# Performance work log

Measured on AMD Instinct MI355X. Metric: run time of the kernel, lower is better.

Reference implementation:

```python
import jax, jax.numpy as jnp
import numpy as np

NUM_HEADS = 16
ROPE_THETA = 10000.0


def _vision_rope_tables(seq_len, head_dim):
    # Llama4 vision ('mllama4') 2D rotary: x/y patch-grid positions,
    # interleaved (non-neox) complex pairs. Returns cos/sin [S, head_dim//2].
    idx = int(np.sqrt(seq_len))  # patches per side (24 for 336/14)
    pos = np.arange(seq_len)
    fx = (pos % idx + 1).astype(np.float32)
    fy = (pos // idx + 1).astype(np.float32)
    freq_dim = head_dim // 2
    rope_freq = 1.0 / ROPE_THETA ** (
        np.arange(0, freq_dim, 2)[: freq_dim // 2].astype(np.float32) / freq_dim
    )
    fx = np.repeat(fx[:, None] * rope_freq[None, :], 2, axis=-1)  # [S, freq_dim]
    fy = np.repeat(fy[:, None] * rope_freq[None, :], 2, axis=-1)
    freqs = np.concatenate([fx, fy], axis=-1)[:, ::2]  # [S, head_dim//2]
    return jnp.asarray(np.cos(freqs)), jnp.asarray(np.sin(freqs))


def _apply_rope(x, cos, sin):
    # x: [B, S, H, D]; even/odd interleaved pairs treated as complex numbers
    B, S, H, D = x.shape
    xr = x.reshape(B, S, H, D // 2, 2)
    x0, x1 = xr[..., 0], xr[..., 1]
    c = cos[None, :, None, :]
    s = sin[None, :, None, :]
    o0 = x0 * c - x1 * s
    o1 = x0 * s + x1 * c
    return jnp.stack([o0, o1], axis=-1).reshape(B, S, H, D)


def setup_inputs() -> dict:
    key = jax.random.key(0)
    ks = jax.random.split(key, 5)
    E = 1408
    B, S = 16, 576
    scale = 0.02
    return {
        "hidden_states": jax.random.normal(ks[0], (B, S, E), dtype=jnp.float32),
        "w_qkv": jax.random.normal(ks[1], (E, 3 * E), dtype=jnp.float32) * scale,
        "b_qkv": jax.random.normal(ks[2], (3 * E,), dtype=jnp.float32) * scale,
        "w_o": jax.random.normal(ks[3], (E, E), dtype=jnp.float32) * scale,
        "b_o": jax.random.normal(ks[4], (E,), dtype=jnp.float32) * scale,
    }


def reference(hidden_states, w_qkv, b_qkv, w_o, b_o):
    B, S, E = hidden_states.shape
    H = NUM_HEADS
    D = E // H
    scaling = D ** -0.5

    qkv = hidden_states @ w_qkv + b_qkv  # [B,S,3E]
    q, k, v = jnp.split(qkv, 3, axis=-1)
    q = q.reshape(B, S, H, D)
    k = k.reshape(B, S, H, D)
    v = v.reshape(B, S, H, D)

    cos, sin = _vision_rope_tables(S, D)
    q = _apply_rope(q, cos, sin)
    k = _apply_rope(k, cos, sin)

    q = q * scaling
    scores = jnp.einsum("bqhd,bkhd->bhqk", q, k)  # full bidirectional attention
    probs = jax.nn.softmax(scores, axis=-1)
    attn = jnp.einsum("bhqk,bkhd->bqhd", probs, v).reshape(B, S, E)

    return attn @ w_o + b_o
```

## Files before the change

kernel.cpp:

```cpp
#include <hip/hip_runtime.h>
#include <hip/hip_bf16.h>


typedef unsigned short UST;
typedef __attribute__((ext_vector_type(8))) __bf16 bf16x8;
typedef __attribute__((ext_vector_type(4))) float f32x4;
typedef __attribute__((ext_vector_type(8))) UST us8;
typedef __attribute__((ext_vector_type(4))) UST us4;

typedef __attribute__((address_space(3))) unsigned int lds_u32;
typedef const __attribute__((address_space(1))) unsigned int glob_u32;

static __device__ __forceinline__ float bf2f(UST u){
  unsigned int x = ((unsigned int)u) << 16;
  return __builtin_bit_cast(float, x);
}
static __device__ __forceinline__ UST f2bf(float f){
  unsigned int x = __builtin_bit_cast(unsigned int, f);
  x += 0x7fffu + ((x >> 16) & 1u);
  return (UST)(x >> 16);
}

__global__ void k_tables(float* __restrict__ cs2){
  int s = blockIdx.x;
  int p = threadIdx.x;
  if (p >= 44) return;
  int tt = p % 22;
  double comp = (p < 22) ? (double)(s % 24 + 1) : (double)(s / 24 + 1);
  double a = comp * pow(10000.0, -(double)tt / 22.0);
  cs2[s*88 + 2*p]     = (float)cos(a);
  cs2[s*88 + 2*p + 1] = (float)sin(a);
}

__global__ void k_zero(UST* __restrict__ qa, UST* __restrict__ ka, UST* __restrict__ vt){
  int c = blockIdx.x*256 + threadIdx.x;
  int bh = c / 576, s = c - bh*576;
  us8 z = {0,0,0,0,0,0,0,0};
  *(us8*)(qa + ((size_t)bh*576 + s)*96 + 88) = z;
  *(us8*)(ka + ((size_t)bh*576 + s)*96 + 88) = z;
  *(us8*)(vt + (size_t)bh*55296 + 50688 + s*8) = z;
}

__global__ void k_cvt(const float* __restrict__ in, UST* __restrict__ out, int n4){
  int i = blockIdx.x * 256 + threadIdx.x;
  if (i >= n4) return;
  float4 v = ((const float4*)in)[i];
  us4 o; o[0]=f2bf(v.x); o[1]=f2bf(v.y); o[2]=f2bf(v.z); o[3]=f2bf(v.w);
  *(us4*)(out + 4*(size_t)i) = o;
}

__global__ void k_cvt_t(const float* __restrict__ W, UST* __restrict__ Bt, int K, int N){
  __shared__ __align__(16) UST tl[64][70];
  int kt = blockIdx.x, nt = blockIdx.y;
  int t = threadIdx.x;
  int k = t >> 2, u = t & 3;
  const float* src = W + (size_t)(kt*64 + k)*N + nt*64 + u*16;
#pragma unroll
  for (int i = 0; i < 4; ++i){
    float4 v = *(const float4*)(src + 4*i);
    UST* d = &tl[k][u*16 + 4*i];
    d[0]=f2bf(v.x); d[1]=f2bf(v.y); d[2]=f2bf(v.z); d[3]=f2bf(v.w);
  }
  __syncthreads();
  int n = t >> 2;
  UST* dst = Bt + (size_t)(nt*64 + n)*K + kt*64 + u*16;
#pragma unroll
  for (int i = 0; i < 2; ++i){
    us8 o;
#pragma unroll
    for (int j = 0; j < 8; ++j) o[j] = tl[u*16 + 8*i + j][n];
    *(us8*)(dst + 8*i) = o;
  }
}

template<int EPI>
__global__ __launch_bounds__(256, 2) void k_gemm(
    const UST* __restrict__ A, const UST* __restrict__ Bt,
    const float* __restrict__ bias, void* __restrict__ Cout,
    int M, int N, int K,
    UST* __restrict__ qa, UST* __restrict__ ka, UST* __restrict__ vt,
    const float* __restrict__ cs2)
{
  __shared__ __align__(16) char SMEM[65536];
  UST (*lA)[128][64] = reinterpret_cast<UST(*)[128][64]>(SMEM);
  UST (*lB)[128][64] = reinterpret_cast<UST(*)[128][64]>(SMEM + 32768);
  float* sm = reinterpret_cast<float*>(SMEM);

  const int t = threadIdx.x;
  const int bm = blockIdx.x, bn = blockIdx.y;
  const int wave = t >> 6, lane = t & 63;
  const int lm = lane & 15, g = lane >> 4;
  const int wr = (wave >> 1) << 6, wc = (wave & 1) << 6;
  const int lrow = lane >> 3;
  const int lcol = (((lane & 7) ^ lrow) << 3);
  const UST* Ag = A  + (size_t)(bm*128 + wave*32 + lrow)*K + lcol;
  const UST* Bg = Bt + (size_t)(bn*128 + wave*32 + lrow)*K + lcol;

  f32x4 zero = {0.f,0.f,0.f,0.f};
  f32x4 acc[4][4];
#pragma unroll
  for (int i=0;i<4;++i)
#pragma unroll
    for (int j=0;j<4;++j) acc[i][j] = zero;

  const int nkt = K >> 6;
  auto stage = [&](int kt, int buf){
#pragma unroll
    for (int c = 0; c < 4; ++c){
      __builtin_amdgcn_global_load_lds((glob_u32*)(Ag + (size_t)kt*64 + (size_t)(8*c)*K),
                                       (lds_u32*)(&lA[buf][wave*32 + 8*c][0]), 16, 0, 0);
      __builtin_amdgcn_global_load_lds((glob_u32*)(Bg + (size_t)kt*64 + (size_t)(8*c)*K),
                                       (lds_u32*)(&lB[buf][wave*32 + 8*c][0]), 16, 0, 0);
    }
  };

  stage(0, 0);
  __syncthreads();
  const int swz = (lm & 7) << 3;

  for (int kt = 0; kt < nkt; ++kt){
    const int cur = kt & 1;
    if (kt + 1 < nkt) stage(kt + 1, cur ^ 1);
#pragma unroll
    for (int ks = 0; ks < 2; ++ks){
      bf16x8 af[4], bfv[4];
      const int cb = (ks*32 + g*8) ^ swz;
#pragma unroll
      for (int mf = 0; mf < 4; ++mf)
        af[mf] = __builtin_bit_cast(bf16x8, *(const us8*)&lA[cur][wr + mf*16 + lm][cb]);
#pragma unroll
      for (int nf = 0; nf < 4; ++nf)
        bfv[nf] = __builtin_bit_cast(bf16x8, *(const us8*)&lB[cur][wc + nf*16 + lm][cb]);
#pragma unroll
      for (int mf = 0; mf < 4; ++mf)
#pragma unroll
        for (int nf = 0; nf < 4; ++nf)
          acc[mf][nf] = __builtin_amdgcn_mfma_f32_16x16x32_bf16(af[mf], bfv[nf], acc[mf][nf], 0, 0, 0);
    }
    __syncthreads();
  }

  if (EPI == 0){
#pragma unroll
    for (int nf = 0; nf < 4; ++nf){
      const int col = bn*128 + wc + nf*16 + lm;
      const float bv = bias[col];
#pragma unroll
      for (int mf = 0; mf < 4; ++mf){
        const size_t rb = (size_t)(bm*128 + wr + mf*16 + g*4);
#pragma unroll
        for (int r = 0; r < 4; ++r)
          ((float*)Cout)[(rb + r)*(size_t)N + col] = acc[mf][nf][r] + bv;
      }
    }
  } else {
#pragma unroll
    for (int nf = 0; nf < 4; ++nf){
      const int col = wc + nf*16 + lm;
      const float bv = bias[bn*128 + col];
#pragma unroll
      for (int mf = 0; mf < 4; ++mf){
#pragma unroll
        for (int r = 0; r < 4; ++r){
          const int row = wr + mf*16 + g*4 + r;
          const int colS = (((col >> 3) ^ (row & 7)) << 3) | (col & 7);
          sm[row*128 + colS] = acc[mf][nf][r] + bv;
        }
      }
    }
    __syncthreads();

    const int j = bn / 11;
    const int bnr = bn - j*11;
    if (j == 2){
#pragma unroll
      for (int i = 0; i < 8; ++i){
        const int idx = t + 256*i;
        const int col = idx & 127, rch = idx >> 7;
        const int cv = bnr*128 + col;
        const int h = cv / 88, dv = cv - h*88;
        const int s0g = bm*128 + rch*8;
        const int b2 = s0g / 576, sl = s0g - b2*576;
        us8 o;
#pragma unroll
        for (int k = 0; k < 8; ++k){
          const int row = rch*8 + k;
          const int colS = (((col >> 3) ^ (row & 7)) << 3) | (col & 7);
          o[k] = f2bf(sm[row*128 + colS]);
        }
        *(us8*)(vt + ((size_t)(b2*16 + h)*96 + dv)*576 + sl) = o;
      }
    } else {
      UST* outp = j ? ka : qa;
      const float sc = j ? 1.0f : 0.10660035817780521f;
#pragma unroll
      for (int i = 0; i < 8; ++i){
        const int idx = t + 256*i;
        const int ch = idx & 15, rr = idx >> 4;
        const int cv = bnr*128 + ch*8;
        const int h = cv / 88, d0 = cv - h*88;
        const int rb = bm*128 + rr;
        const int b2 = rb / 576, s = rb - b2*576;
        const float* src = &sm[rr*128 + ((ch ^ (rr & 7)) << 3)];
        float x[8];
#pragma unroll
        for (int k = 0; k < 8; ++k) x[k] = src[k];
        const float* tb = cs2 + s*88 + d0;
        float4 q0 = *(const float4*)(tb);
        float4 q1 = *(const float4*)(tb + 4);
        float cc[4]  = {q0.x, q0.z, q1.x, q1.z};
        float ssv[4] = {q0.y, q0.w, q1.y, q1.w};
        us8 o;
#pragma unroll
        for (int p = 0; p < 4; ++p){
          float o0 = (x[2*p]*cc[p]  - x[2*p+1]*ssv[p]) * sc;
          float o1 = (x[2*p]*ssv[p] + x[2*p+1]*cc[p])  * sc;
          o[2*p] = f2bf(o0); o[2*p+1] = f2bf(o1);
        }
        *(us8*)(outp + ((size_t)(b2*16 + h)*576 + s)*96 + d0) = o;
      }
    }
  }
}

__global__ __launch_bounds__(256, 2) void k_attn(
    const UST* __restrict__ qa, const UST* __restrict__ ka,
    const UST* __restrict__ vt, UST* __restrict__ outp)
{
  __shared__ __align__(16) UST lK[64][104];
  __shared__ __align__(16) UST lV[96][72];
  __shared__ __align__(16) UST lP[4][16][72];
  const int bh = blockIdx.x, qt = blockIdx.y;
  const int t = threadIdx.x, wave = t >> 6, lane = t & 63;
  const int lm = lane & 15, g = lane >> 4;
  const int h = bh & 15, b = bh >> 4;

  bf16x8 qf[3];
  {
    const UST* qp = qa + ((size_t)bh*576 + qt*64 + wave*16 + lm)*96 + g*8;
#pragma unroll
    for (int ks = 0; ks < 3; ++ks) qf[ks] = __builtin_bit_cast(bf16x8, *(const us8*)(qp + ks*32));
  }
  f32x4 zero = {0.f,0.f,0.f,0.f};
  f32x4 acc[6];
#pragma unroll
  for (int i = 0; i < 6; ++i) acc[i] = zero;
  float psum[4];
#pragma unroll
  for (int r = 0; r < 4; ++r) psum[r] = 0.f;

  const UST* kbase = ka + (size_t)bh*576*96;
  const UST* vbase = vt + (size_t)bh*96*576;

  for (int kvt = 0; kvt < 9; ++kvt){
    {
      int r = t >> 2, u = t & 3;
      const UST* src = kbase + (size_t)(kvt*64 + r)*96 + u*24;
#pragma unroll
      for (int i = 0; i < 3; ++i)
        *(uint4*)&lK[r][u*24 + i*8] = *(const uint4*)(src + i*8);
    }
    if (t < 192){
      int d = t >> 1, hf = t & 1;
      const UST* src = vbase + (size_t)d*576 + kvt*64 + hf*32;
#pragma unroll
      for (int i = 0; i < 4; ++i)
        *(uint4*)&lV[d][hf*32 + i*8] = *(const uint4*)(src + i*8);
    }
    __syncthreads();

    f32x4 sc[4];
#pragma unroll
    for (int i = 0; i < 4; ++i) sc[i] = zero;
    __builtin_amdgcn_s_setprio(1);
#pragma unroll
    for (int ks = 0; ks < 3; ++ks){
#pragma unroll
      for (int nf = 0; nf < 4; ++nf){
        bf16x8 kf = __builtin_bit_cast(bf16x8, *(const us8*)&lK[nf*16 + lm][ks*32 + g*8]);
        sc[nf] = __builtin_amdgcn_mfma_f32_16x16x32_bf16(qf[ks], kf, sc[nf], 0, 0, 0);
      }
    }
    __builtin_amdgcn_s_setprio(0);

#pragma unroll
    for (int r = 0; r < 4; ++r){
      float ls = 0.f;
#pragma unroll
      for (int nf = 0; nf < 4; ++nf){
        float p = __expf(sc[nf][r]);
        sc[nf][r] = p;
        ls += p;
      }
      psum[r] += ls;
    }

#pragma unroll
    for (int nf = 0; nf < 4; ++nf)
#pragma unroll
      for (int r = 0; r < 4; ++r)
        lP[wave][4*g + r][nf*16 + lm] = f2bf(sc[nf][r]);

    bf16x8 pa[2];
#pragma unroll
    for (int ks2 = 0; ks2 < 2; ++ks2)
      pa[ks2] = __builtin_bit_cast(bf16x8, *(const us8*)&lP[wave][lm][ks2*32 + g*8]);
    __builtin_amdgcn_s_setprio(1);
#pragma unroll
    for (int ks2 = 0; ks2 < 2; ++ks2)
#pragma unroll
      for (int df = 0; df < 6; ++df){
        bf16x8 vf = __builtin_bit_cast(bf16x8, *(const us8*)&lV[df*16 + lm][ks2*32 + g*8]);
        acc[df] = __builtin_amdgcn_mfma_f32_16x16x32_bf16(pa[ks2], vf, acc[df], 0, 0, 0);
      }
    __builtin_amdgcn_s_setprio(0);
    __syncthreads();
  }

#pragma unroll
  for (int m = 1; m <= 8; m <<= 1)
#pragma unroll
    for (int r = 0; r < 4; ++r) psum[r] += __shfl_xor(psum[r], m, 64);
  float inv[4];
#pragma unroll
  for (int r = 0; r < 4; ++r) inv[r] = 1.f / psum[r];

  const size_t rowt = (size_t)b*576 + qt*64 + wave*16;
#pragma unroll
  for (int df = 0; df < 6; ++df){
    int d = df*16 + lm;
    if (d < 88){
#pragma unroll
      for (int r = 0; r < 4; ++r)
        outp[(rowt + 4*g + r)*1408 + h*88 + d] = f2bf(acc[df][r] * inv[r]);
    }
  }
}

extern "C" void kernel_launch(void* const* d_in, const int* in_sizes, int n_in,
                              void* d_out, int out_size, void* d_ws, size_t ws_size,
                              hipStream_t stream)
{
  (void)in_sizes; (void)n_in; (void)out_size; (void)ws_size;
  const float* hs   = (const float*)d_in[0];
  const float* wqkv = (const float*)d_in[1];
  const float* bqkv = (const float*)d_in[2];
  const float* wo   = (const float*)d_in[3];
  const float* bo   = (const float*)d_in[4];
  float* out = (float*)d_out;

  char* w = (char*)d_ws;
  UST* A_bf   = (UST*)(w);
  UST* Bt1    = (UST*)(w + 25952256);
  UST* Bt2    = (UST*)(w + 37847040);
  UST* qa     = (UST*)(w + 41811968);
  UST* ka     = (UST*)(w + 70123520);
  UST* vt     = (UST*)(w + 98435072);
  float* cs2  = (float*)(w + 126746624);

  k_tables<<<576, 64, 0, stream>>>(cs2);
  k_zero<<<576, 256, 0, stream>>>(qa, ka, vt);
  k_cvt<<<12672, 256, 0, stream>>>(hs, A_bf, 3244032);
  k_cvt_t<<<dim3(22, 66), 256, 0, stream>>>(wqkv, Bt1, 1408, 4224);
  k_cvt_t<<<dim3(22, 22), 256, 0, stream>>>(wo, Bt2, 1408, 1408);
  k_gemm<3><<<dim3(72, 33), 256, 0, stream>>>(A_bf, Bt1, bqkv, nullptr, 9216, 4224, 1408,
                                              qa, ka, vt, cs2);
  k_attn<<<dim3(256, 9), 256, 0, stream>>>(qa, ka, vt, A_bf);
  k_gemm<0><<<dim3(72, 11), 256, 0, stream>>>(A_bf, Bt2, bo, out, 9216, 1408, 1408,
                                              nullptr, nullptr, nullptr, nullptr);
}
```

Measured before the change: 293.0 us.

## Use 256x256 direct-to-LDS pipelined GEMM for output projection; prefetch attention K/V tiles

Replaces the 128x128 output-projection GEMM with a 512-thread, 256x256-tile kernel. It double-buffers tiles loaded straight into LDS with global_load_lds and splits each k-step into quarter phases. The weight transpose pads N to 1536 with zero rows to fit the larger tiles. Attention now prefetches the next K/V tile into registers while computing on the current one. The larger tile gives more reuse, but the grid drops to 216 blocks, fewer than the CU count, and the padded columns add wasted work.

```diff
diff --git a/kernel.cpp b/kernel.cpp
--- a/kernel.cpp
+++ b/kernel.cpp
@@ -53,7 +53,15 @@
   __shared__ __align__(16) UST tl[64][70];
   int kt = blockIdx.x, nt = blockIdx.y;
   int t = threadIdx.x;
-  int k = t >> 2, u = t & 3;
+  int u = t & 3;
+  int n = t >> 2;
+  UST* dst = Bt + (size_t)(nt*64 + n)*K + kt*64 + u*16;
+  if (nt*64 >= N){
+    us8 z = {0,0,0,0,0,0,0,0};
+    *(us8*)(dst) = z; *(us8*)(dst + 8) = z;
+    return;
+  }
+  int k = t >> 2;
   const float* src = W + (size_t)(kt*64 + k)*N + nt*64 + u*16;
 #pragma unroll
   for (int i = 0; i < 4; ++i){
@@ -62,8 +70,6 @@
     d[0]=f2bf(v.x); d[1]=f2bf(v.y); d[2]=f2bf(v.z); d[3]=f2bf(v.w);
   }
   __syncthreads();
-  int n = t >> 2;
-  UST* dst = Bt + (size_t)(nt*64 + n)*K + kt*64 + u*16;
 #pragma unroll
   for (int i = 0; i < 2; ++i){
     us8 o;
@@ -73,10 +79,9 @@
   }
 }
 
-template<int EPI>
-__global__ __launch_bounds__(256, 2) void k_gemm(
+__global__ __launch_bounds__(256, 2) void k_gemmqkv(
     const UST* __restrict__ A, const UST* __restrict__ Bt,
-    const float* __restrict__ bias, void* __restrict__ Cout,
+    const float* __restrict__ bias,
     int M, int N, int K,
     UST* __restrict__ qa, UST* __restrict__ ka, UST* __restrict__ vt,
     const float* __restrict__ cs2)
@@ -140,92 +145,178 @@
     __syncthreads();
   }
 
-  if (EPI == 0){
-#pragma unroll
-    for (int nf = 0; nf < 4; ++nf){
-      const int col = bn*128 + wc + nf*16 + lm;
-      const float bv = bias[col];
-#pragma unroll
-      for (int mf = 0; mf < 4; ++mf){
-        const size_t rb = (size_t)(bm*128 + wr + mf*16 + g*4);
-#pragma unroll
-        for (int r = 0; r < 4; ++r)
-          ((float*)Cout)[(rb + r)*(size_t)N + col] = acc[mf][nf][r] + bv;
-      }
+#pragma unroll
+  for (int nf = 0; nf < 4; ++nf){
+    const int col = wc + nf*16 + lm;
+    const float bv = bias[bn*128 + col];
+#pragma unroll
+    for (int mf = 0; mf < 4; ++mf){
+#pragma unroll
+      for (int r = 0; r < 4; ++r){
+        const int row = wr + mf*16 + g*4 + r;
+        const int colS = (((col >> 3) ^ (row & 7)) << 3) | (col & 7);
+        sm[row*128 + colS] = acc[mf][nf][r] + bv;
+      }
+    }
+  }
+  __syncthreads();
+
+  const int j = bn / 11;
+  const int bnr = bn - j*11;
+  if (j == 2){
+#pragma unroll
+    for (int i = 0; i < 8; ++i){
+      const int idx = t + 256*i;
+      const int col = idx & 127, rch = idx >> 7;
+      const int cv = bnr*128 + col;
+      const int h = cv / 88, dv = cv - h*88;
+      const int s0g = bm*128 + rch*8;
+      const int b2 = s0g / 576, sl = s0g - b2*576;
+      us8 o;
+#pragma unroll
+      for (int k = 0; k < 8; ++k){
+        const int row = rch*8 + k;
+        const int colS = (((col >> 3) ^ (row & 7)) << 3) | (col & 7);
+        o[k] = f2bf(sm[row*128 + colS]);
+      }
+      *(us8*)(vt + ((size_t)(b2*16 + h)*96 + dv)*576 + sl) = o;
     }
   } else {
-#pragma unroll
-    for (int nf = 0; nf < 4; ++nf){
-      const int col = wc + nf*16 + lm;
-      const float bv = bias[bn*128 + col];
-#pragma unroll
-      for (int mf = 0; mf < 4; ++mf){
-#pragma unroll
-        for (int r = 0; r < 4; ++r){
-          const int row = wr + mf*16 + g*4 + r;
-          const int colS = (((col >> 3) ^ (row & 7)) << 3) | (col & 7);
-          sm[row*128 + colS] = acc[mf][nf][r] + bv;
-        }
-      }
-    }
-    __syncthreads();
-
-    const int j = bn / 11;
-    const int bnr = bn - j*11;
-    if (j == 2){
-#pragma unroll
-      for (int i = 0; i < 8; ++i){
-        const int idx = t + 256*i;
-        const int col = idx & 127, rch = idx >> 7;
-        const int cv = bnr*128 + col;
-        const int h = cv / 88, dv = cv - h*88;
-        const int s0g = bm*128 + rch*8;
-        const int b2 = s0g / 576, sl = s0g - b2*576;
-        us8 o;
-#pragma unroll
-        for (int k = 0; k < 8; ++k){
-          const int row = rch*8 + k;
-          const int colS = (((col >> 3) ^ (row & 7)) << 3) | (col & 7);
-          o[k] = f2bf(sm[row*128 + colS]);
-        }
-        *(us8*)(vt + ((size_t)(b2*16 + h)*96 + dv)*576 + sl) = o;
-      }
-    } else {
-      UST* outp = j ? ka : qa;
-      const float sc = j ? 1.0f : 0.10660035817780521f;
-#pragma unroll
-      for (int i = 0; i < 8; ++i){
-        const int idx = t + 256*i;
-        const int ch = idx & 15, rr = idx >> 4;
-        const int cv = bnr*128 + ch*8;
-        const int h = cv / 88, d0 = cv - h*88;
-        const int rb = bm*128 + rr;
-        const int b2 = rb / 576, s = rb - b2*576;
-        const float* src = &sm[rr*128 + ((ch ^ (rr & 7)) << 3)];
-        float x[8];
-#pragma unroll
-        for (int k = 0; k < 8; ++k) x[k] = src[k];
-        const float* tb = cs2 + s*88 + d0;
-        float4 q0 = *(const float4*)(tb);
-        float4 q1 = *(const float4*)(tb + 4);
-        float cc[4]  = {q0.x, q0.z, q1.x, q1.z};
-        float ssv[4] = {q0.y, q0.w, q1.y, q1.w};
-        us8 o;
-#pragma unroll
-        for (int p = 0; p < 4; ++p){
-          float o0 = (x[2*p]*cc[p]  - x[2*p+1]*ssv[p]) * sc;
-          float o1 = (x[2*p]*ssv[p] + x[2*p+1]*cc[p])  * sc;
-          o[2*p] = f2bf(o0); o[2*p+1] = f2bf(o1);
-        }
-        *(us8*)(outp + ((size_t)(b2*16 + h)*576 + s)*96 + d0) = o;
-      }
+    UST* outp = j ? ka : qa;
+    const float sc = j ? 1.0f : 0.10660035817780521f;
+#pragma unroll
+    for (int i = 0; i < 8; ++i){
+      const int idx = t + 256*i;
+      const int ch = idx & 15, rr = idx >> 4;
+      const int cv = bnr*128 + ch*8;
+      const int h = cv / 88, d0 = cv - h*88;
+      const int rb = bm*128 + rr;
+      const int b2 = rb / 576, s = rb - b2*576;
+      const float* src = &sm[rr*128 + ((ch ^ (rr & 7)) << 3)];
+      float x[8];
+#pragma unroll
+      for (int k = 0; k < 8; ++k) x[k] = src[k];
+      const float* tb = cs2 + s*88 + d0;
+      float4 q0 = *(const float4*)(tb);
+      float4 q1 = *(const float4*)(tb + 4);
+      float cc[4]  = {q0.x, q0.z, q1.x, q1.z};
+      float ssv[4] = {q0.y, q0.w, q1.y, q1.w};
+      us8 o;
+#pragma unroll
+      for (int p = 0; p < 4; ++p){
+        float o0 = (x[2*p]*cc[p]  - x[2*p+1]*ssv[p]) * sc;
+        float o1 = (x[2*p]*ssv[p] + x[2*p+1]*cc[p])  * sc;
+        o[2*p] = f2bf(o0); o[2*p+1] = f2bf(o1);
+      }
+      *(us8*)(outp + ((size_t)(b2*16 + h)*576 + s)*96 + d0) = o;
+    }
+  }
+}
+
+__global__ __launch_bounds__(512, 1) void k_gemm8p(
+    const UST* __restrict__ A, const UST* __restrict__ Bt,
+    const float* __restrict__ bias, float* __restrict__ C,
+    int M, int N, int K)
+{
+  __shared__ __align__(16) UST lA[2][256][64];
+  __shared__ __align__(16) UST lB[2][256][64];
+  const int t = threadIdx.x;
+  const int wave = t >> 6, lane = t & 63;
+  const int lm = lane & 15, g = lane >> 4;
+  const int wm = wave >> 2, wn = wave & 3;
+  const int bm = blockIdx.x, bn = blockIdx.y;
+  const int nkt = K >> 6;
+
+  const int lr8 = lane >> 3;
+  const int schunk = ((lane & 7) ^ lr8) << 3;
+
+  auto stage = [&](int tt2, int h){
+    const int s = tt2 & 1;
+    const int rb0 = (h & 1)*128 + wave*8;
+    const UST* src = (h < 2) ? A : Bt;
+    const int base = ((h < 2) ? bm : bn)*256;
+#pragma unroll
+    for (int j = 0; j < 2; ++j){
+      const int rl = rb0 + j*64;
+      UST* ldst = (h < 2) ? &lA[s][rl][0] : &lB[s][rl][0];
+      __builtin_amdgcn_global_load_lds(
+        (glob_u32*)(src + (size_t)(base + rl + lr8)*K + tt2*64 + schunk),
+        (lds_u32*)ldst, 16, 0, 0);
+    }
+  };
+
+  f32x4 zero = {0.f,0.f,0.f,0.f};
+  f32x4 acc[8][4];
+#pragma unroll
+  for (int i=0;i<8;++i)
+#pragma unroll
+    for (int j=0;j<4;++j) acc[i][j] = zero;
+
+#pragma unroll
+  for (int h = 0; h < 4; ++h) stage(0, h);
+
+  const int sw7 = lm & 7;
+
+  for (int tt = 0; tt < nkt; ++tt){
+    const int s = tt & 1;
+#pragma unroll
+    for (int q = 0; q < 4; ++q){
+      if (tt + 1 < nkt) stage(tt + 1, q);
+      if (q == 0){
+        if (tt + 1 < nkt) asm volatile("s_waitcnt vmcnt(2)" ::: "memory");
+        else              asm volatile("s_waitcnt vmcnt(0)" ::: "memory");
+        __builtin_amdgcn_sched_barrier(0);
+      }
+      __builtin_amdgcn_s_barrier();
+
+      const int qm = q >> 1, qn = q & 1;
+      bf16x8 af[4][2], bfr[2][2];
+#pragma unroll
+      for (int ks = 0; ks < 2; ++ks){
+        const int cb = (((ks << 2) | g) ^ sw7) << 3;
+#pragma unroll
+        for (int mf = 0; mf < 4; ++mf)
+          af[mf][ks] = __builtin_bit_cast(bf16x8,
+            *(const us8*)&lA[s][wm*128 + (qm*4 + mf)*16 + lm][cb]);
+#pragma unroll
+        for (int nf = 0; nf < 2; ++nf)
+          bfr[nf][ks] = __builtin_bit_cast(bf16x8,
+            *(const us8*)&lB[s][wn*64 + (qn*2 + nf)*16 + lm][cb]);
+      }
+      __builtin_amdgcn_s_setprio(1);
+#pragma unroll
+      for (int mf = 0; mf < 4; ++mf)
+#pragma unroll
+        for (int nf = 0; nf < 2; ++nf)
+#pragma unroll
+          for (int ks = 0; ks < 2; ++ks)
+            acc[qm*4 + mf][qn*2 + nf] =
+              __builtin_amdgcn_mfma_f32_16x16x32_bf16(af[mf][ks], bfr[nf][ks],
+                                                      acc[qm*4 + mf][qn*2 + nf], 0, 0, 0);
+      __builtin_amdgcn_s_setprio(0);
+      __builtin_amdgcn_s_barrier();
+    }
+  }
+
+#pragma unroll
+  for (int nf = 0; nf < 4; ++nf){
+    const int col = bn*256 + wn*64 + nf*16 + lm;
+    if (col >= N) continue;
+    const float bv = bias[col];
+#pragma unroll
+    for (int mf = 0; mf < 8; ++mf){
+      const size_t rb = (size_t)(bm*256 + wm*128 + mf*16 + g*4);
+#pragma unroll
+      for (int r = 0; r < 4; ++r)
+        C[(rb + r)*(size_t)N + col] = acc[mf][nf][r] + bv;
     }
   }
 }
 
 __global__ __launch_bounds__(256, 2) void k_attn(
     const UST* __restrict__ qa, const UST* __restrict__ ka,
-    const UST* __restrict__ vt, UST* __restrict__ outp)
+    const UST* __restrict__ vt, const UST* __restrict__ outp_dummy,
+    UST* __restrict__ outp)
 {
   __shared__ __align__(16) UST lK[64][104];
   __shared__ __align__(16) UST lV[96][72];
@@ -252,22 +343,32 @@
   const UST* kbase = ka + (size_t)bh*576*96;
   const UST* vbase = vt + (size_t)bh*96*576;
 
+  const int rK = t >> 2, uK = t & 3;
+  const int dV = t >> 1, hfV = t & 1;
+  const UST* ksrc = kbase + (size_t)rK*96 + uK*24;
+  const UST* vsrc = vbase + (size_t)dV*576 + hfV*32;
+  uint4 kreg[3], vreg[4];
+  auto loadrs = [&](int kvt){
+#pragma unroll
+    for (int i = 0; i < 3; ++i)
+      kreg[i] = *(const uint4*)(ksrc + (size_t)kvt*6144 + i*8);
+    if (t < 192){
+#pragma unroll
+      for (int i = 0; i < 4; ++i)
+        vreg[i] = *(const uint4*)(vsrc + kvt*64 + i*8);
+    }
+  };
+  loadrs(0);
+
   for (int kvt = 0; kvt < 9; ++kvt){
-    {
-      int r = t >> 2, u = t & 3;
-      const UST* src = kbase + (size_t)(kvt*64 + r)*96 + u*24;
-#pragma unroll
-      for (int i = 0; i < 3; ++i)
-        *(uint4*)&lK[r][u*24 + i*8] = *(const uint4*)(src + i*8);
-    }
+#pragma unroll
+    for (int i = 0; i < 3; ++i) *(uint4*)&lK[rK][uK*24 + i*8] = kreg[i];
     if (t < 192){
-      int d = t >> 1, hf = t & 1;
-      const UST* src = vbase + (size_t)d*576 + kvt*64 + hf*32;
-#pragma unroll
-      for (int i = 0; i < 4; ++i)
-        *(uint4*)&lV[d][hf*32 + i*8] = *(const uint4*)(src + i*8);
+#pragma unroll
+      for (int i = 0; i < 4; ++i) *(uint4*)&lV[dV][hfV*32 + i*8] = vreg[i];
     }
     __syncthreads();
+    if (kvt + 1 < 9) loadrs(kvt + 1);
 
     f32x4 sc[4];
 #pragma unroll
@@ -353,19 +454,18 @@
   UST* A_bf   = (UST*)(w);
   UST* Bt1    = (UST*)(w + 25952256);
   UST* Bt2    = (UST*)(w + 37847040);
-  UST* qa     = (UST*)(w + 41811968);
-  UST* ka     = (UST*)(w + 70123520);
-  UST* vt     = (UST*)(w + 98435072);
-  float* cs2  = (float*)(w + 126746624);
+  UST* qa     = (UST*)(w + 42172416);
+  UST* ka     = (UST*)(w + 70483968);
+  UST* vt     = (UST*)(w + 98795520);
+  float* cs2  = (float*)(w + 127107072);
 
   k_tables<<<576, 64, 0, stream>>>(cs2);
   k_zero<<<576, 256, 0, stream>>>(qa, ka, vt);
   k_cvt<<<12672, 256, 0, stream>>>(hs, A_bf, 3244032);
   k_cvt_t<<<dim3(22, 66), 256, 0, stream>>>(wqkv, Bt1, 1408, 4224);
-  k_cvt_t<<<dim3(22, 22), 256, 0, stream>>>(wo, Bt2, 1408, 1408);
-  k_gemm<3><<<dim3(72, 33), 256, 0, stream>>>(A_bf, Bt1, bqkv, nullptr, 9216, 4224, 1408,
+  k_cvt_t<<<dim3(22, 24), 256, 0, stream>>>(wo, Bt2, 1408, 1408);
+  k_gemmqkv<<<dim3(72, 33), 256, 0, stream>>>(A_bf, Bt1, bqkv, 9216, 4224, 1408,
                                               qa, ka, vt, cs2);
-  k_attn<<<dim3(256, 9), 256, 0, stream>>>(qa, ka, vt, A_bf);
-  k_gemm<0><<<dim3(72, 11), 256, 0, stream>>>(A_bf, Bt2, bo, out, 9216, 1408, 1408,
-                                              nullptr, nullptr, nullptr, nullptr);
-}
+  k_attn<<<dim3(256, 9), 256, 0, stream>>>(qa, ka, vt, nullptr, A_bf);
+  k_gemm8p<<<dim3(36, 6), 512, 0, stream>>>(A_bf, Bt2, bo, out, 9216, 1408, 1408);
+}
```

Result: slower. 460.7 us (+57.2%).
